# Optimization experiments

Hardware: AMD Instinct MI355X
Metric: run time of the kernel (lower is better)

The kernel has to match this reference:

```python
import jax, jax.numpy as jnp
import numpy as np
from jax import lax

N, E, F, H, B = 16384, 262144, 32, 128, 16
DI, DS, DC, DTR = 256, 16, 4, 8   # Mamba: d_inner=expand*H, d_state, d_conv, dt_rank=ceil(H/16)
NS, NC = 512, 8                   # num_stations, num line colors
EPS = 1e-5


def _forward(node_features, edge_index, batch, W_in, b_in, W_g1, b_g1, W_g2, b_g2,
             W_inproj, conv_w, conv_b, W_xproj, W_dt, b_dt, A_log, D_p, W_out,
             gamma, beta, Wc, bc, Wh, bh, Wt, bt, Wp1, bp1, Wp2, bp2, Wd, bd, Ws, bs):
    def gcn(x, W, b):
        # GCNConv with self-loops and symmetric normalization
        loops = jnp.arange(N)
        s = jnp.concatenate([edge_index[0], loops])
        d = jnp.concatenate([edge_index[1], loops])
        deg = jax.ops.segment_sum(jnp.ones(s.shape[0], x.dtype), d, num_segments=N)
        dinv = jnp.where(deg > 0, lax.rsqrt(deg), 0.0)
        xw = x @ W
        msg = xw[s] * (dinv[s] * dinv[d])[:, None]
        return jax.ops.segment_sum(msg, d, num_segments=N) + b

    h = jax.nn.relu(node_features @ W_in + b_in)
    h = jax.nn.relu(gcn(h, W_g1, b_g1))
    h_gnn = jax.nn.relu(gcn(h, W_g2, b_g2))

    # --- Mamba block over the node sequence (batch dim of 1, seq_len = N) ---
    xz = h_gnn @ W_inproj                      # (N, 2*DI)
    x, z = xz[:, :DI], xz[:, DI:]
    xp = jnp.pad(x, ((DC - 1, 0), (0, 0)))     # causal depthwise conv1d
    xc = conv_b + sum(xp[k:k + N] * conv_w[:, k] for k in range(DC))
    x = jax.nn.silu(xc)
    dbl = x @ W_xproj                          # (N, DTR + 2*DS)
    dt = jax.nn.softplus(dbl[:, :DTR] @ W_dt + b_dt)   # (N, DI)
    Bm = dbl[:, DTR:DTR + DS]                  # (N, DS)
    Cm = dbl[:, DTR + DS:]                     # (N, DS)
    A = -jnp.exp(A_log)                        # (DI, DS)
    dA = jnp.exp(dt[:, :, None] * A[None])     # (N, DI, DS)
    dBx = dt[:, :, None] * Bm[:, None, :] * x[:, :, None]

    def step(hst, t):
        dA_t, dBx_t, C_t = t
        hst = dA_t * hst + dBx_t               # (DI, DS)
        return hst, hst @ C_t                  # (DI,)

    _, ys = lax.scan(step, jnp.zeros((DI, DS), x.dtype), (dA, dBx, Cm))
    y = (ys + D_p * x) * jax.nn.silu(z)
    h_mamba = y @ W_out                        # (N, H)

    # residual + LayerNorm
    hh = h_gnn + h_mamba
    mu = hh.mean(-1, keepdims=True)
    var = ((hh - mu) ** 2).mean(-1, keepdims=True)
    h_final = (hh - mu) * lax.rsqrt(var + EPS) * gamma + beta

    # global_mean_pool per graph
    counts = jax.ops.segment_sum(jnp.ones(N, h_final.dtype), batch, num_segments=B)
    ge = jax.ops.segment_sum(h_final, batch, num_segments=B) / jnp.maximum(counts, 1.0)[:, None]

    # critic + all policy heads, concatenated: [1,4,3,NS,NS,NS,NC]
    return jnp.concatenate([ge @ Wc + bc, ge @ Wh + bh, ge @ Wt + bt,
                            ge @ Wp1 + bp1, ge @ Wp2 + bp2, ge @ Wd + bd,
                            ge @ Ws + bs], axis=-1)


def setup_inputs() -> dict:
    key = jax.random.key(0)
    ks = list(jax.random.split(key, 20))
    p = lambda i, shape, s=0.02: jax.random.normal(ks[i], shape, jnp.float32) * s
    return dict(
        node_features=jax.random.normal(ks[0], (N, F), jnp.float32),
        edge_index=jax.random.randint(ks[1], (2, E), 0, N),
        batch=jnp.sort(jax.random.randint(ks[2], (N,), 0, B)),
        W_in=p(3, (F, H)), b_in=jnp.zeros((H,), jnp.float32),
        W_g1=p(4, (H, H)), b_g1=jnp.zeros((H,), jnp.float32),
        W_g2=p(5, (H, H)), b_g2=jnp.zeros((H,), jnp.float32),
        W_inproj=p(6, (H, 2 * DI)),
        conv_w=p(7, (DI, DC)), conv_b=jnp.zeros((DI,), jnp.float32),
        W_xproj=p(8, (DI, DTR + 2 * DS)),
        W_dt=p(9, (DTR, DI)), b_dt=jnp.full((DI,), -4.0, jnp.float32),
        A_log=jnp.log(jnp.broadcast_to(jnp.arange(1.0, DS + 1.0, dtype=jnp.float32), (DI, DS))),
        D_p=jnp.ones((DI,), jnp.float32),
        W_out=p(10, (DI, H)),
        gamma=jnp.ones((H,), jnp.float32), beta=jnp.zeros((H,), jnp.float32),
        Wc=p(11, (H, 1)), bc=jnp.zeros((1,), jnp.float32),
        Wh=p(12, (H, 4)), bh=jnp.zeros((4,), jnp.float32),
        Wt=p(13, (H, 3)), bt=jnp.zeros((3,), jnp.float32),
        Wp1=p(14, (H, NS)), bp1=jnp.zeros((NS,), jnp.float32),
        Wp2=p(15, (H, NS)), bp2=jnp.zeros((NS,), jnp.float32),
        Wd=p(16, (H, NS)), bd=jnp.zeros((NS,), jnp.float32),
        Ws=p(17, (H, NC)), bs=jnp.zeros((NC,), jnp.float32),
    )


def reference(node_features, edge_index, batch, W_in, b_in, W_g1, b_g1, W_g2, b_g2,
              W_inproj, conv_w, conv_b, W_xproj, W_dt, b_dt, A_log, D_p, W_out,
              gamma, beta, Wc, bc, Wh, bh, Wt, bt, Wp1, bp1, Wp2, bp2, Wd, bd, Ws, bs):
    return _forward(node_features, edge_index, batch, W_in, b_in, W_g1, b_g1, W_g2, b_g2,
                    W_inproj, conv_w, conv_b, W_xproj, W_dt, b_dt, A_log, D_p, W_out,
                    gamma, beta, Wc, bc, Wh, bh, Wt, bt, Wp1, bp1, Wp2, bp2, Wd, bd, Ws, bs)
```

## Files before the change

kernel.cpp:

```cpp
#include <hip/hip_runtime.h>
#include <math.h>

#define NN 16384
#define EE 262144
#define FF 32
#define HH 128
#define BB 16
#define DI 256
#define DS 16
#define DC 4
#define DTR 8
#define OUTW 1552
#define NCH 256
#define CHLEN 64

__device__ __forceinline__ float siluf(float v) { return v / (1.f + __expf(-v)); }
__device__ __forceinline__ float softplusf(float v) {
    return fmaxf(v, 0.f) + __logf(1.f + __expf(-fabsf(v)));
}

__global__ void zero_kernel(int* __restrict__ cnt, float* __restrict__ ge,
                            int* __restrict__ counts) {
    int idx = blockIdx.x * blockDim.x + threadIdx.x;
    if (idx < NN) cnt[idx] = 0;
    if (idx < BB * HH) ge[idx] = 0.f;
    if (idx < BB) counts[idx] = 0;
}

__global__ void deg_kernel(const int* __restrict__ dst, int* __restrict__ cnt) {
    int e = blockIdx.x * blockDim.x + threadIdx.x;
    if (e < EE) atomicAdd(&cnt[dst[e]], 1);
}

__global__ __launch_bounds__(1024) void prefix_kernel(const int* __restrict__ cnt,
                                                      int* __restrict__ rowptr,
                                                      int* __restrict__ cursor,
                                                      float* __restrict__ dinv) {
    __shared__ int part[1024];
    int tid = threadIdx.x;
    int4 c4[4];
#pragma unroll
    for (int j = 0; j < 4; j++) c4[j] = ((const int4*)cnt)[tid * 4 + j];
    int v[16] = {c4[0].x, c4[0].y, c4[0].z, c4[0].w, c4[1].x, c4[1].y, c4[1].z, c4[1].w,
                 c4[2].x, c4[2].y, c4[2].z, c4[2].w, c4[3].x, c4[3].y, c4[3].z, c4[3].w};
    int s = 0;
#pragma unroll
    for (int j = 0; j < 16; j++) s += v[j];
    part[tid] = s;
    __syncthreads();
    for (int off = 1; off < 1024; off <<= 1) {
        int t = (tid >= off) ? part[tid - off] : 0;
        __syncthreads();
        part[tid] += t;
        __syncthreads();
    }
    int running = part[tid] - s;
    int rp[16];
    float dv[16];
#pragma unroll
    for (int j = 0; j < 16; j++) {
        rp[j] = running;
        running += v[j];
        dv[j] = rsqrtf((float)(v[j] + 1));
    }
#pragma unroll
    for (int j = 0; j < 4; j++) {
        int4 r4; r4.x = rp[j*4]; r4.y = rp[j*4+1]; r4.z = rp[j*4+2]; r4.w = rp[j*4+3];
        ((int4*)rowptr)[tid * 4 + j] = r4;
        ((int4*)cursor)[tid * 4 + j] = r4;
        float4 d4; d4.x = dv[j*4]; d4.y = dv[j*4+1]; d4.z = dv[j*4+2]; d4.w = dv[j*4+3];
        ((float4*)dinv)[tid * 4 + j] = d4;
    }
    if (tid == 1023) rowptr[NN] = part[1023];
}

__global__ void scatter_kernel(const int* __restrict__ src, const int* __restrict__ dst,
                               int* __restrict__ cursor, int* __restrict__ col) {
    int e = blockIdx.x * blockDim.x + threadIdx.x;
    if (e < EE) {
        int d = dst[e];
        int pos = atomicAdd(&cursor[d], 1);
        col[pos] = src[e];
    }
}

__global__ __launch_bounds__(256) void gemm_k(const float* __restrict__ A,
                                              const float* __restrict__ B,
                                              const float* __restrict__ bias,
                                              float* __restrict__ C,
                                              int M, int Nn, int K, int act) {
    __shared__ float As[16][68];
    __shared__ float Bs[16][68];
    int tid = threadIdx.x;
    int m0 = blockIdx.y * 64;
    int n0 = blockIdx.x * 64;
    int ty = tid >> 4, tx = tid & 15;
    float acc[4][4] = {{0.f}};
    for (int k0 = 0; k0 < K; k0 += 16) {
#pragma unroll
        for (int l = 0; l < 4; l++) {
            int idx = tid + l * 256;
            int i = idx >> 4, j = idx & 15;
            As[j][i] = A[(size_t)(m0 + i) * K + k0 + j];
        }
#pragma unroll
        for (int l = 0; l < 4; l++) {
            int idx = tid + l * 256;
            int i = idx >> 6, j = idx & 63;
            int n = n0 + j;
            Bs[i][j] = (n < Nn) ? B[(size_t)(k0 + i) * Nn + n] : 0.f;
        }
        __syncthreads();
#pragma unroll
        for (int kk = 0; kk < 16; kk++) {
            float4 a4 = *(const float4*)&As[kk][ty * 4];
            float4 b4 = *(const float4*)&Bs[kk][tx * 4];
            float av[4] = {a4.x, a4.y, a4.z, a4.w};
            float bv[4] = {b4.x, b4.y, b4.z, b4.w};
#pragma unroll
            for (int r = 0; r < 4; r++)
#pragma unroll
                for (int c = 0; c < 4; c++) acc[r][c] = fmaf(av[r], bv[c], acc[r][c]);
        }
        __syncthreads();
    }
    int nb = n0 + tx * 4;
    if (nb < Nn) {
        float4 bi4 = {0.f, 0.f, 0.f, 0.f};
        if (bias) bi4 = *(const float4*)&bias[nb];
#pragma unroll
        for (int r = 0; r < 4; r++) {
            int m = m0 + ty * 4 + r;
            float4 v;
            v.x = acc[r][0] + bi4.x; v.y = acc[r][1] + bi4.y;
            v.z = acc[r][2] + bi4.z; v.w = acc[r][3] + bi4.w;
            if (act == 1) {
                v.x = fmaxf(v.x, 0.f); v.y = fmaxf(v.y, 0.f);
                v.z = fmaxf(v.z, 0.f); v.w = fmaxf(v.w, 0.f);
            }
            *(float4*)&C[(size_t)m * Nn + nb] = v;
        }
    }
}

__global__ __launch_bounds__(512, 4) void gemm_big512(const float* __restrict__ A,
                                                      const float* __restrict__ B,
                                                      float* __restrict__ C,
                                                      int M, int Nn, int K) {
    __shared__ float As[16][132];
    __shared__ float Bs[16][132];
    int tid = threadIdx.x;
    int m0 = blockIdx.y * 128;
    int n0 = blockIdx.x * 128;
    int ty = tid >> 4;
    int tx = tid & 15;
    float acc[4][8] = {{0.f}};
    for (int k0 = 0; k0 < K; k0 += 16) {
        {
            int m = tid >> 2;
            int kc = (tid & 3) * 4;
            float4 a = *(const float4*)&A[(size_t)(m0 + m) * K + k0 + kc];
            As[kc + 0][m] = a.x; As[kc + 1][m] = a.y;
            As[kc + 2][m] = a.z; As[kc + 3][m] = a.w;
        }
        {
            int krow = tid >> 5;
            int c4 = (tid & 31) * 4;
            *(float4*)&Bs[krow][c4] = *(const float4*)&B[(size_t)(k0 + krow) * Nn + n0 + c4];
        }
        __syncthreads();
#pragma unroll
        for (int kk = 0; kk < 16; kk++) {
            float4 a4 = *(const float4*)&As[kk][ty * 4];
            float4 b0 = *(const float4*)&Bs[kk][tx * 4];
            float4 b1 = *(const float4*)&Bs[kk][64 + tx * 4];
            float av[4] = {a4.x, a4.y, a4.z, a4.w};
            float bv[8] = {b0.x, b0.y, b0.z, b0.w, b1.x, b1.y, b1.z, b1.w};
#pragma unroll
            for (int r = 0; r < 4; r++)
#pragma unroll
                for (int c = 0; c < 8; c++) acc[r][c] = fmaf(av[r], bv[c], acc[r][c]);
        }
        __syncthreads();
    }
#pragma unroll
    for (int r = 0; r < 4; r++) {
        int m = m0 + ty * 4 + r;
        float4 v0, v1;
        v0.x = acc[r][0]; v0.y = acc[r][1]; v0.z = acc[r][2]; v0.w = acc[r][3];
        v1.x = acc[r][4]; v1.y = acc[r][5]; v1.z = acc[r][6]; v1.w = acc[r][7];
        *(float4*)&C[(size_t)m * Nn + n0 + tx * 4] = v0;
        *(float4*)&C[(size_t)m * Nn + n0 + 64 + tx * 4] = v1;
    }
}

__global__ __launch_bounds__(256) void gemm_at_dblt(const float* __restrict__ AT,
                                                    const float* __restrict__ B,
                                                    float* __restrict__ dblt) {
    __shared__ float As[16][68];
    __shared__ float Bs[16][68];
    __shared__ float Ct[64][41];
    int tid = threadIdx.x;
    int m0 = blockIdx.x * 64;
    int ty = tid >> 4, tx = tid & 15;
    float acc[4][4] = {{0.f}};
    for (int k0 = 0; k0 < DI; k0 += 16) {
#pragma unroll
        for (int l = 0; l < 4; l++) {
            int idx = tid + l * 256;
            int kk = idx >> 6, i = idx & 63;
            As[kk][i] = AT[(size_t)(k0 + kk) * NN + m0 + i];
        }
#pragma unroll
        for (int l = 0; l < 4; l++) {
            int idx = tid + l * 256;
            int i = idx >> 6, j = idx & 63;
            Bs[i][j] = (j < 40) ? B[(size_t)(k0 + i) * 40 + j] : 0.f;
        }
        __syncthreads();
#pragma unroll
        for (int kk = 0; kk < 16; kk++) {
            float4 a4 = *(const float4*)&As[kk][ty * 4];
            float4 b4 = *(const float4*)&Bs[kk][tx * 4];
            float av[4] = {a4.x, a4.y, a4.z, a4.w};
            float bv[4] = {b4.x, b4.y, b4.z, b4.w};
#pragma unroll
            for (int r = 0; r < 4; r++)
#pragma unroll
                for (int c = 0; c < 4; c++) acc[r][c] = fmaf(av[r], bv[c], acc[r][c]);
        }
        __syncthreads();
    }
    if (tx * 4 < 40) {
#pragma unroll
        for (int r = 0; r < 4; r++) {
            int m = ty * 4 + r;
            Ct[m][tx * 4 + 0] = acc[r][0];
            Ct[m][tx * 4 + 1] = acc[r][1];
            Ct[m][tx * 4 + 2] = acc[r][2];
            Ct[m][tx * 4 + 3] = acc[r][3];
        }
    }
    __syncthreads();
#pragma unroll
    for (int l = 0; l < 10; l++) {
        int idx = tid + l * 256;
        int n = idx >> 6, m = idx & 63;
        dblt[(size_t)n * NN + m0 + m] = Ct[m][n];
    }
}

__global__ __launch_bounds__(256) void gemm_at_ln(const float* __restrict__ AT,
                                                  const float* __restrict__ B,
                                                  const float* __restrict__ hg,
                                                  const float* __restrict__ gamma,
                                                  const float* __restrict__ beta,
                                                  float* __restrict__ out) {
    __shared__ float As[16][36];
    __shared__ float Bs[16][132];
    int tid = threadIdx.x;
    int m0 = blockIdx.x * 32;
    int ty = tid >> 4, tx = tid & 15;
    float acc[2][8] = {{0.f}};
    for (int k0 = 0; k0 < 256; k0 += 16) {
        {
            int idx = tid * 2;
            int kk = idx >> 5, i = idx & 31;
            As[kk][i] = AT[(size_t)(k0 + kk) * NN + m0 + i];
            As[kk][i + 1] = AT[(size_t)(k0 + kk) * NN + m0 + i + 1];
        }
        {
            int krow = tid >> 4;
            int c8 = (tid & 15) * 8;
            const float* bp = &B[(size_t)(k0 + krow) * HH + c8];
            *(float4*)&Bs[krow][c8] = *(const float4*)bp;
            *(float4*)&Bs[krow][c8 + 4] = *(const float4*)(bp + 4);
        }
        __syncthreads();
#pragma unroll
        for (int kk = 0; kk < 16; kk++) {
            float a0 = As[kk][ty * 2];
            float a1 = As[kk][ty * 2 + 1];
            float4 b0 = *(const float4*)&Bs[kk][tx * 4];
            float4 b1 = *(const float4*)&Bs[kk][64 + tx * 4];
            float bv[8] = {b0.x, b0.y, b0.z, b0.w, b1.x, b1.y, b1.z, b1.w};
#pragma unroll
            for (int c = 0; c < 8; c++) {
                acc[0][c] = fmaf(a0, bv[c], acc[0][c]);
                acc[1][c] = fmaf(a1, bv[c], acc[1][c]);
            }
        }
        __syncthreads();
    }
    float4 g0 = *(const float4*)&gamma[tx * 4];
    float4 g1 = *(const float4*)&gamma[64 + tx * 4];
    float4 be0 = *(const float4*)&beta[tx * 4];
    float4 be1 = *(const float4*)&beta[64 + tx * 4];
    float gv[8] = {g0.x, g0.y, g0.z, g0.w, g1.x, g1.y, g1.z, g1.w};
    float bv[8] = {be0.x, be0.y, be0.z, be0.w, be1.x, be1.y, be1.z, be1.w};
#pragma unroll
    for (int r = 0; r < 2; r++) {
        int m = m0 + ty * 2 + r;
        float4 h0 = *(const float4*)&hg[(size_t)m * HH + tx * 4];
        float4 h1 = *(const float4*)&hg[(size_t)m * HH + 64 + tx * 4];
        float v[8] = {acc[r][0] + h0.x, acc[r][1] + h0.y, acc[r][2] + h0.z, acc[r][3] + h0.w,
                      acc[r][4] + h1.x, acc[r][5] + h1.y, acc[r][6] + h1.z, acc[r][7] + h1.w};
        float sum = 0.f;
#pragma unroll
        for (int c = 0; c < 8; c++) sum += v[c];
        sum += __shfl_xor(sum, 1); sum += __shfl_xor(sum, 2);
        sum += __shfl_xor(sum, 4); sum += __shfl_xor(sum, 8);
        float mu = sum * (1.f / 128.f);
        float vs = 0.f;
#pragma unroll
        for (int c = 0; c < 8; c++) { float dd = v[c] - mu; vs += dd * dd; }
        vs += __shfl_xor(vs, 1); vs += __shfl_xor(vs, 2);
        vs += __shfl_xor(vs, 4); vs += __shfl_xor(vs, 8);
        float inv = rsqrtf(vs * (1.f / 128.f) + 1e-5f);
        float4 o0, o1;
        o0.x = (v[0] - mu) * inv * gv[0] + bv[0];
        o0.y = (v[1] - mu) * inv * gv[1] + bv[1];
        o0.z = (v[2] - mu) * inv * gv[2] + bv[2];
        o0.w = (v[3] - mu) * inv * gv[3] + bv[3];
        o1.x = (v[4] - mu) * inv * gv[4] + bv[4];
        o1.y = (v[5] - mu) * inv * gv[5] + bv[5];
        o1.z = (v[6] - mu) * inv * gv[6] + bv[6];
        o1.w = (v[7] - mu) * inv * gv[7] + bv[7];
        *(float4*)&out[(size_t)m * HH + tx * 4] = o0;
        *(float4*)&out[(size_t)m * HH + 64 + tx * 4] = o1;
    }
}

__global__ __launch_bounds__(256) void gcn_gather4(const float* __restrict__ xw,
                                                   const int* __restrict__ rowptr,
                                                   const int* __restrict__ col,
                                                   const float* __restrict__ dinv,
                                                   const float* __restrict__ b,
                                                   float* __restrict__ out) {
    int tid = threadIdx.x;
    int sub = tid & 31;
    int n = blockIdx.x * 8 + (tid >> 5);
    float dn = dinv[n];
    const float4* xw4 = (const float4*)xw;
    float4 a = xw4[(size_t)n * 32 + sub];
    float ws = dn * dn;
    float4 acc;
    acc.x = a.x * ws; acc.y = a.y * ws; acc.z = a.z * ws; acc.w = a.w * ws;
    int beg = rowptr[n], end = rowptr[n + 1];
    int e = beg;
    for (; e + 4 <= end; e += 4) {
        int s0 = col[e], s1 = col[e + 1], s2 = col[e + 2], s3 = col[e + 3];
        float w0 = dinv[s0] * dn, w1 = dinv[s1] * dn;
        float w2 = dinv[s2] * dn, w3 = dinv[s3] * dn;
        float4 v0 = xw4[(size_t)s0 * 32 + sub];
        float4 v1 = xw4[(size_t)s1 * 32 + sub];
        float4 v2 = xw4[(size_t)s2 * 32 + sub];
        float4 v3 = xw4[(size_t)s3 * 32 + sub];
        acc.x = fmaf(v0.x, w0, acc.x); acc.y = fmaf(v0.y, w0, acc.y);
        acc.z = fmaf(v0.z, w0, acc.z); acc.w = fmaf(v0.w, w0, acc.w);
        acc.x = fmaf(v1.x, w1, acc.x); acc.y = fmaf(v1.y, w1, acc.y);
        acc.z = fmaf(v1.z, w1, acc.z); acc.w = fmaf(v1.w, w1, acc.w);
        acc.x = fmaf(v2.x, w2, acc.x); acc.y = fmaf(v2.y, w2, acc.y);
        acc.z = fmaf(v2.z, w2, acc.z); acc.w = fmaf(v2.w, w2, acc.w);
        acc.x = fmaf(v3.x, w3, acc.x); acc.y = fmaf(v3.y, w3, acc.y);
        acc.z = fmaf(v3.z, w3, acc.z); acc.w = fmaf(v3.w, w3, acc.w);
    }
    for (; e < end; e++) {
        int s0 = col[e];
        float w0 = dinv[s0] * dn;
        float4 v0 = xw4[(size_t)s0 * 32 + sub];
        acc.x = fmaf(v0.x, w0, acc.x); acc.y = fmaf(v0.y, w0, acc.y);
        acc.z = fmaf(v0.z, w0, acc.z); acc.w = fmaf(v0.w, w0, acc.w);
    }
    float4 b4 = ((const float4*)b)[sub];
    acc.x = fmaxf(acc.x + b4.x, 0.f);
    acc.y = fmaxf(acc.y + b4.y, 0.f);
    acc.z = fmaxf(acc.z + b4.z, 0.f);
    acc.w = fmaxf(acc.w + b4.w, 0.f);
    ((float4*)out)[(size_t)n * 32 + sub] = acc;
}

__global__ __launch_bounds__(256) void conv_silu_t(const float* __restrict__ xz,
                                                   const float* __restrict__ cw,
                                                   const float* __restrict__ cb,
                                                   float* __restrict__ xst,
                                                   float* __restrict__ szt) {
    __shared__ float tile[67][65];
    int tid = threadIdx.x;
    int t0 = blockIdx.x * 64;
    int c0 = blockIdx.y * 64;
#pragma unroll
    for (int l = 0; l < 17; l++) {
        int idx = tid + l * 256;
        if (idx < 67 * 64) {
            int r = idx >> 6, c = idx & 63;
            int gt = t0 - 3 + r;
            tile[r][c] = (gt >= 0) ? xz[(size_t)gt * 512 + c0 + c] : 0.f;
        }
    }
    __syncthreads();
    int tl = tid & 63;
    int d0 = tid >> 6;
    if (c0 < 256) {
#pragma unroll
        for (int l = 0; l < 16; l++) {
            int dl = d0 + l * 4;
            int dg = c0 + dl;
            float acc = cb[dg];
#pragma unroll
            for (int k = 0; k < DC; k++)
                acc = fmaf(tile[tl + k][dl], cw[dg * DC + k], acc);
            xst[dg * NN + t0 + tl] = siluf(acc);
        }
    } else {
#pragma unroll
        for (int l = 0; l < 16; l++) {
            int dl = d0 + l * 4;
            int dg = c0 - 256 + dl;
            szt[dg * NN + t0 + tl] = siluf(tile[tl + 3][dl]);
        }
    }
}

__global__ __launch_bounds__(256, 6) void scan_phase1(const float* __restrict__ xst,
                                                      const float* __restrict__ dblt,
                                                      const float* __restrict__ A_log,
                                                      const float* __restrict__ W_dt,
                                                      const float* __restrict__ b_dt,
                                                      float* __restrict__ chkP,
                                                      float* __restrict__ chkH) {
    __shared__ float Td[32][68];
    __shared__ float Tx[32][68];
    __shared__ float Bs[16][68];
    __shared__ float D8[8][68];
    int tid = threadIdx.x;
    int wave = tid >> 6, lane = tid & 63;
    int sg = lane & 7, dl = lane >> 3;
    int dblk = blockIdx.x, chunk = blockIdx.y;
    int t0 = chunk * CHLEN;
    int dloc = wave * 8 + dl;
    int d = dblk * 32 + dloc;
    int s0 = 2 * sg;
#pragma unroll
    for (int p = 0; p < 2; p++) {
        int linear = tid + p * 256;
        int row = linear >> 4, c4 = (linear & 15) * 4;
        *(float4*)&Tx[row][c4] = *(const float4*)&xst[(size_t)(dblk * 32 + row) * NN + t0 + c4];
    }
    if (tid < 128) {
        int r = tid >> 4, c4 = (tid & 15) * 4;
        *(float4*)&D8[r][c4] = *(const float4*)&dblt[(size_t)r * NN + t0 + c4];
    }
    {
        int s = tid >> 4, c4 = (tid & 15) * 4;
        *(float4*)&Bs[s][c4] = *(const float4*)&dblt[(size_t)(8 + s) * NN + t0 + c4];
    }
    float A0 = -expf(A_log[d * DS + s0]);
    float A1 = -expf(A_log[d * DS + s0 + 1]);
    __syncthreads();
    {
        int row = tid >> 3;
        int tb = (tid & 7) * 8;
        int dd = dblk * 32 + row;
        float bd = b_dt[dd];
        float wv[8];
#pragma unroll
        for (int j = 0; j < 8; j++) wv[j] = W_dt[j * DI + dd];
#pragma unroll
        for (int j = 0; j < 8; j++) {
            int t = tb + j;
            float acc = bd;
#pragma unroll
            for (int k = 0; k < 8; k++) acc = fmaf(D8[k][t], wv[k], acc);
            Td[row][t] = softplusf(acc);
        }
    }
    __syncthreads();
    float h0 = 0.f, h1 = 0.f, P0 = 1.f, P1 = 1.f;
    for (int i = 0; i < CHLEN; i += 4) {
        float4 d4 = *(const float4*)&Td[dloc][i];
        float4 x4 = *(const float4*)&Tx[dloc][i];
        float4 b04 = *(const float4*)&Bs[s0][i];
        float4 b14 = *(const float4*)&Bs[s0 + 1][i];
#define P1S(U) { float dtv = d4.U; float a0 = __expf(dtv * A0); float a1 = __expf(dtv * A1); \
        float dx = dtv * x4.U; h0 = fmaf(a0, h0, dx * b04.U); h1 = fmaf(a1, h1, dx * b14.U); \
        P0 *= a0; P1 *= a1; }
        P1S(x) P1S(y) P1S(z) P1S(w)
#undef P1S
    }
    int idx = chunk * 4096 + d * DS + s0;
    float2 vP; vP.x = P0; vP.y = P1;
    float2 vH; vH.x = h0; vH.y = h1;
    *(float2*)(chkP + idx) = vP;
    *(float2*)(chkH + idx) = vH;
}

__global__ void scan_phase2(const float* __restrict__ chkP, const float* __restrict__ chkH,
                            float* __restrict__ init) {
    int idx = blockIdx.x * blockDim.x + threadIdx.x;
    float h = 0.f;
    for (int c0 = 0; c0 < NCH; c0 += 8) {
        float p[8], q[8];
#pragma unroll
        for (int j = 0; j < 8; j++) {
            p[j] = chkP[(c0 + j) * 4096 + idx];
            q[j] = chkH[(c0 + j) * 4096 + idx];
        }
#pragma unroll
        for (int j = 0; j < 8; j++) {
            init[(c0 + j) * 4096 + idx] = h;
            h = fmaf(p[j], h, q[j]);
        }
    }
}

__global__ __launch_bounds__(256, 6) void scan_phase3(const float* __restrict__ xst,
                                                      const float* __restrict__ dblt,
                                                      const float* __restrict__ A_log,
                                                      const float* __restrict__ W_dt,
                                                      const float* __restrict__ b_dt,
                                                      const float* __restrict__ init,
                                                      const float* __restrict__ D_p,
                                                      const float* __restrict__ szt,
                                                      float* __restrict__ yt) {
    __shared__ float Td[32][68];
    __shared__ float Tx[32][68];
    __shared__ float Bs[16][68];
    __shared__ float CsD8[16][68];
    int tid = threadIdx.x;
    int wave = tid >> 6, lane = tid & 63;
    int sg = lane & 7, dl = lane >> 3;
    int dblk = blockIdx.x, chunk = blockIdx.y;
    int t0 = chunk * CHLEN;
    int dloc = wave * 8 + dl;
    int d = dblk * 32 + dloc;
    int s0 = 2 * sg;
#pragma unroll
    for (int p = 0; p < 2; p++) {
        int linear = tid + p * 256;
        int row = linear >> 4, c4 = (linear & 15) * 4;
        *(float4*)&Tx[row][c4] = *(const float4*)&xst[(size_t)(dblk * 32 + row) * NN + t0 + c4];
    }
    if (tid < 128) {
        int r = tid >> 4, c4 = (tid & 15) * 4;
        *(float4*)&CsD8[r][c4] = *(const float4*)&dblt[(size_t)r * NN + t0 + c4];
    }
    {
        int s = tid >> 4, c4 = (tid & 15) * 4;
        *(float4*)&Bs[s][c4] = *(const float4*)&dblt[(size_t)(8 + s) * NN + t0 + c4];
    }
    float A0 = -expf(A_log[d * DS + s0]);
    float A1 = -expf(A_log[d * DS + s0 + 1]);
    float Dd = D_p[d];
    float2 ini = *(const float2*)(init + chunk * 4096 + d * DS + s0);
    float h0 = ini.x, h1 = ini.y;
    __syncthreads();
    {
        int row = tid >> 3;
        int tb = (tid & 7) * 8;
        int dd = dblk * 32 + row;
        float bd = b_dt[dd];
        float wv[8];
#pragma unroll
        for (int j = 0; j < 8; j++) wv[j] = W_dt[j * DI + dd];
#pragma unroll
        for (int j = 0; j < 8; j++) {
            int t = tb + j;
            float acc = bd;
#pragma unroll
            for (int k = 0; k < 8; k++) acc = fmaf(CsD8[k][t], wv[k], acc);
            Td[row][t] = softplusf(acc);
        }
    }
    __syncthreads();
    {
        int s = tid >> 4, c4 = (tid & 15) * 4;
        *(float4*)&CsD8[s][c4] = *(const float4*)&dblt[(size_t)(24 + s) * NN + t0 + c4];
    }
    float szv[8];
#pragma unroll
    for (int r = 0; r < 8; r++)
        szv[r] = szt[(size_t)(dblk * 32 + wave * 8 + r) * NN + t0 + lane];
    __syncthreads();
    for (int i = 0; i < CHLEN; i += 4) {
        float4 d4 = *(const float4*)&Td[dloc][i];
        float4 x4 = *(const float4*)&Tx[dloc][i];
        float4 b04 = *(const float4*)&Bs[s0][i];
        float4 b14 = *(const float4*)&Bs[s0 + 1][i];
        float4 c04 = *(const float4*)&CsD8[s0][i];
        float4 c14 = *(const float4*)&CsD8[s0 + 1][i];
        float4 yv;
#define P3S(U) { float dtv = d4.U; float a0 = __expf(dtv * A0); float a1 = __expf(dtv * A1); \
        float dx = dtv * x4.U; h0 = fmaf(a0, h0, dx * b04.U); h1 = fmaf(a1, h1, dx * b14.U); \
        float c = fmaf(h1, c14.U, h0 * c04.U); \
        c += __shfl_xor(c, 1); c += __shfl_xor(c, 2); c += __shfl_xor(c, 4); \
        yv.U = c + Dd * x4.U; }
        P3S(x) P3S(y) P3S(z) P3S(w)
#undef P3S
        if (sg == 0) *(float4*)&Td[dloc][i] = yv;
    }
#pragma unroll
    for (int r = 0; r < 8; r++) {
        int row = wave * 8 + r;
        yt[(size_t)(dblk * 32 + row) * NN + t0 + lane] = Td[row][lane] * szv[r];
    }
}

__global__ void pool_kernel(const float* __restrict__ hf, const int* __restrict__ batch,
                            float* __restrict__ ge, int* __restrict__ counts) {
    int f = threadIdx.x;
    int r0 = blockIdx.x * 64;
    int gcur = batch[r0];
    float acc = 0.f;
    int cnt = 0;
    for (int i = 0; i < 64; i += 4) {
        int r = r0 + i;
        int g0 = batch[r], g3 = batch[r + 3];
        float v0 = hf[(size_t)r * HH + f];
        float v1 = hf[(size_t)(r + 1) * HH + f];
        float v2 = hf[(size_t)(r + 2) * HH + f];
        float v3 = hf[(size_t)(r + 3) * HH + f];
        if (g0 == gcur && g3 == gcur) {
            acc += (v0 + v1) + (v2 + v3);
            cnt += 4;
        } else {
            int gs[4] = {g0, batch[r + 1], batch[r + 2], g3};
            float vs[4] = {v0, v1, v2, v3};
#pragma unroll
            for (int k = 0; k < 4; k++) {
                if (gs[k] != gcur) {
                    atomicAdd(&ge[gcur * HH + f], acc);
                    if (f == 0) atomicAdd(&counts[gcur], cnt);
                    acc = 0.f; cnt = 0; gcur = gs[k];
                }
                acc += vs[k];
                cnt++;
            }
        }
    }
    atomicAdd(&ge[gcur * HH + f], acc);
    if (f == 0) atomicAdd(&counts[gcur], cnt);
}

__global__ void heads_kernel(const float* __restrict__ ge, const int* __restrict__ counts,
                             const float* Wc, const float* bc, const float* Wh, const float* bh,
                             const float* Wt, const float* bt, const float* Wp1, const float* bp1,
                             const float* Wp2, const float* bp2, const float* Wd, const float* bd,
                             const float* Ws, const float* bs, float* __restrict__ out) {
    int col = blockIdx.x * blockDim.x + threadIdx.x;
    int b = blockIdx.y;
    if (col >= OUTW) return;
    const float* W; const float* bi; int lc, w;
    if (col < 1)         { W = Wc;  bi = bc;  lc = col;        w = 1; }
    else if (col < 5)    { W = Wh;  bi = bh;  lc = col - 1;    w = 4; }
    else if (col < 8)    { W = Wt;  bi = bt;  lc = col - 5;    w = 3; }
    else if (col < 520)  { W = Wp1; bi = bp1; lc = col - 8;    w = 512; }
    else if (col < 1032) { W = Wp2; bi = bp2; lc = col - 520;  w = 512; }
    else if (col < 1544) { W = Wd;  bi = bd;  lc = col - 1032; w = 512; }
    else                 { W = Ws;  bi = bs;  lc = col - 1544; w = 8; }
    float scale = 1.f / fmaxf((float)counts[b], 1.f);
    float dot = 0.f;
#pragma unroll 8
    for (int f = 0; f < HH; f++) dot = fmaf(ge[b * HH + f], W[f * w + lc], dot);
    out[(size_t)b * OUTW + col] = bi[lc] + scale * dot;
}

extern "C" void kernel_launch(void* const* d_in, const int* in_sizes, int n_in,
                              void* d_out, int out_size, void* d_ws, size_t ws_size,
                              hipStream_t stream) {
    const float* nf      = (const float*)d_in[0];
    const int*   ei      = (const int*)d_in[1];
    const int*   batch   = (const int*)d_in[2];
    const float* W_in    = (const float*)d_in[3];
    const float* b_in    = (const float*)d_in[4];
    const float* W_g1    = (const float*)d_in[5];
    const float* b_g1    = (const float*)d_in[6];
    const float* W_g2    = (const float*)d_in[7];
    const float* b_g2    = (const float*)d_in[8];
    const float* W_inproj= (const float*)d_in[9];
    const float* conv_w  = (const float*)d_in[10];
    const float* conv_b  = (const float*)d_in[11];
    const float* W_xproj = (const float*)d_in[12];
    const float* W_dt    = (const float*)d_in[13];
    const float* b_dt    = (const float*)d_in[14];
    const float* A_log   = (const float*)d_in[15];
    const float* D_p     = (const float*)d_in[16];
    const float* W_out   = (const float*)d_in[17];
    const float* gamma   = (const float*)d_in[18];
    const float* beta    = (const float*)d_in[19];
    const float* Wc = (const float*)d_in[20]; const float* bc = (const float*)d_in[21];
    const float* Wh = (const float*)d_in[22]; const float* bh = (const float*)d_in[23];
    const float* Wt = (const float*)d_in[24]; const float* bt = (const float*)d_in[25];
    const float* Wp1= (const float*)d_in[26]; const float* bp1= (const float*)d_in[27];
    const float* Wp2= (const float*)d_in[28]; const float* bp2= (const float*)d_in[29];
    const float* Wd = (const float*)d_in[30]; const float* bd = (const float*)d_in[31];
    const float* Ws = (const float*)d_in[32]; const float* bs = (const float*)d_in[33];

    const int* e_src = ei;
    const int* e_dst = ei + EE;

    float* w = (float*)d_ws;
    size_t o = 0;
    float* F0   = w + o; o += (size_t)NN * HH;
    float* F1   = w + o; o += (size_t)NN * HH;
    float* F2   = w + o; o += (size_t)NN * HH;
    float* XZ   = w + o; o += (size_t)NN * 512;
    float* YT   = XZ;
    float* XST  = w + o; o += (size_t)NN * DI;
    float* SZT  = w + o; o += (size_t)NN * DI;
    float* DBLT = w + o; o += (size_t)NN * 40;
    float* GE   = w + o; o += BB * HH;
    float* DINV = w + o; o += NN;
    int* ip = (int*)(w + o);
    int* CNT    = ip; ip += NN;
    int* ROWPTR = ip; ip += NN + 1;
    int* CURSOR = ip; ip += NN;
    int* COL    = ip; ip += EE;
    int* COUNTS = ip; ip += BB;

    float* CHP  = F0;
    float* CHH  = F0 + (size_t)NCH * 4096;
    float* INI  = F1;

    zero_kernel<<<(NN + 255) / 256, 256, 0, stream>>>(CNT, GE, COUNTS);

    deg_kernel<<<EE / 256, 256, 0, stream>>>(e_dst, CNT);
    prefix_kernel<<<1, 1024, 0, stream>>>(CNT, ROWPTR, CURSOR, DINV);
    scatter_kernel<<<EE / 256, 256, 0, stream>>>(e_src, e_dst, CURSOR, COL);

    gemm_k<<<dim3(2, NN / 64), 256, 0, stream>>>(nf, W_in, b_in, F0, NN, HH, FF, 1);
    gemm_k<<<dim3(2, NN / 64), 256, 0, stream>>>(F0, W_g1, nullptr, F1, NN, HH, HH, 0);
    gcn_gather4<<<NN / 8, 256, 0, stream>>>(F1, ROWPTR, COL, DINV, b_g1, F0);
    gemm_k<<<dim3(2, NN / 64), 256, 0, stream>>>(F0, W_g2, nullptr, F1, NN, HH, HH, 0);
    gcn_gather4<<<NN / 8, 256, 0, stream>>>(F1, ROWPTR, COL, DINV, b_g2, F2);

    gemm_big512<<<dim3(4, NN / 128), 512, 0, stream>>>(F2, W_inproj, XZ, NN, 512, HH);
    conv_silu_t<<<dim3(NN / 64, 8), 256, 0, stream>>>(XZ, conv_w, conv_b, XST, SZT);
    gemm_at_dblt<<<NN / 64, 256, 0, stream>>>(XST, W_xproj, DBLT);

    scan_phase1<<<dim3(8, NCH), 256, 0, stream>>>(XST, DBLT, A_log, W_dt, b_dt, CHP, CHH);
    scan_phase2<<<16, 256, 0, stream>>>(CHP, CHH, INI);
    scan_phase3<<<dim3(8, NCH), 256, 0, stream>>>(XST, DBLT, A_log, W_dt, b_dt, INI, D_p, SZT, YT);

    gemm_at_ln<<<NN / 32, 256, 0, stream>>>(YT, W_out, F2, gamma, beta, F0);

    pool_kernel<<<NN / 64, HH, 0, stream>>>(F0, batch, GE, COUNTS);

    heads_kernel<<<dim3((OUTW + 127) / 128, BB), 128, 0, stream>>>(
        GE, COUNTS, Wc, bc, Wh, bh, Wt, bt, Wp1, bp1, Wp2, bp2, Wd, bd, Ws, bs, (float*)d_out);
}
```

Before: 403.7 us.

## Write in_proj output transposed, simplify conv, fuse mean-pool into LayerNorm GEMM

The in_proj GEMM now writes its result in channel-major (transposed) layout, so the causal conv+SiLU becomes a simple row-wise vectorized kernel with no shared-memory transpose tile. Separately, the graph mean-pool is fused into the output-projection+LayerNorm kernel: normalized rows are staged in shared memory and reduced per graph with atomics, which removes the F0 write and re-read and one launch. The transposed stores from the GEMM are float4 but strided by NN, which may be less coalesced, and the fused kernel uses more shared memory.

```diff
diff --git a/kernel.cpp b/kernel.cpp
--- a/kernel.cpp
+++ b/kernel.cpp
@@ -143,10 +143,10 @@
     }
 }
 
-__global__ __launch_bounds__(512, 4) void gemm_big512(const float* __restrict__ A,
-                                                      const float* __restrict__ B,
-                                                      float* __restrict__ C,
-                                                      int M, int Nn, int K) {
+__global__ __launch_bounds__(512, 4) void gemm_big512_t(const float* __restrict__ A,
+                                                        const float* __restrict__ B,
+                                                        float* __restrict__ CT,
+                                                        int M, int Nn, int K) {
     __shared__ float As[16][132];
     __shared__ float Bs[16][132];
     int tid = threadIdx.x;
@@ -184,13 +184,42 @@
         __syncthreads();
     }
 #pragma unroll
-    for (int r = 0; r < 4; r++) {
-        int m = m0 + ty * 4 + r;
-        float4 v0, v1;
-        v0.x = acc[r][0]; v0.y = acc[r][1]; v0.z = acc[r][2]; v0.w = acc[r][3];
-        v1.x = acc[r][4]; v1.y = acc[r][5]; v1.z = acc[r][6]; v1.w = acc[r][7];
-        *(float4*)&C[(size_t)m * Nn + n0 + tx * 4] = v0;
-        *(float4*)&C[(size_t)m * Nn + n0 + 64 + tx * 4] = v1;
+    for (int cc = 0; cc < 4; cc++) {
+        float4 v;
+        v.x = acc[0][cc]; v.y = acc[1][cc]; v.z = acc[2][cc]; v.w = acc[3][cc];
+        *(float4*)&CT[(size_t)(n0 + tx * 4 + cc) * NN + m0 + ty * 4] = v;
+        float4 u;
+        u.x = acc[0][cc + 4]; u.y = acc[1][cc + 4]; u.z = acc[2][cc + 4]; u.w = acc[3][cc + 4];
+        *(float4*)&CT[(size_t)(n0 + 64 + tx * 4 + cc) * NN + m0 + ty * 4] = u;
+    }
+}
+
+__global__ __launch_bounds__(256) void conv_silu_rows(const float* __restrict__ xzt,
+                                                      const float* __restrict__ cw,
+                                                      const float* __restrict__ cb,
+                                                      float* __restrict__ xst,
+                                                      float* __restrict__ szt) {
+    int d = blockIdx.y;
+    int tg = blockIdx.x * 1024 + threadIdx.x * 4;
+    const float* row = xzt + (size_t)d * NN;
+    float4 cur = *(const float4*)&row[tg];
+    if (d < DI) {
+        float4 prev;
+        if (tg == 0) { prev.x = 0.f; prev.y = 0.f; prev.z = 0.f; prev.w = 0.f; }
+        else prev = *(const float4*)&row[tg - 4];
+        float w0 = cw[d * DC + 0], w1 = cw[d * DC + 1];
+        float w2 = cw[d * DC + 2], w3 = cw[d * DC + 3];
+        float b = cb[d];
+        float4 o;
+        o.x = siluf(b + w0 * prev.y + w1 * prev.z + w2 * prev.w + w3 * cur.x);
+        o.y = siluf(b + w0 * prev.z + w1 * prev.w + w2 * cur.x + w3 * cur.y);
+        o.z = siluf(b + w0 * prev.w + w1 * cur.x + w2 * cur.y + w3 * cur.z);
+        o.w = siluf(b + w0 * cur.x + w1 * cur.y + w2 * cur.z + w3 * cur.w);
+        *(float4*)&xst[(size_t)d * NN + tg] = o;
+    } else {
+        float4 o;
+        o.x = siluf(cur.x); o.y = siluf(cur.y); o.z = siluf(cur.z); o.w = siluf(cur.w);
+        *(float4*)&szt[(size_t)(d - DI) * NN + tg] = o;
     }
 }
 
@@ -250,14 +279,18 @@
     }
 }
 
-__global__ __launch_bounds__(256) void gemm_at_ln(const float* __restrict__ AT,
-                                                  const float* __restrict__ B,
-                                                  const float* __restrict__ hg,
-                                                  const float* __restrict__ gamma,
-                                                  const float* __restrict__ beta,
-                                                  float* __restrict__ out) {
+__global__ __launch_bounds__(256) void gemm_at_ln_pool(const float* __restrict__ AT,
+                                                       const float* __restrict__ B,
+                                                       const float* __restrict__ hg,
+                                                       const float* __restrict__ gamma,
+                                                       const float* __restrict__ beta,
+                                                       const int* __restrict__ batch,
+                                                       float* __restrict__ ge,
+                                                       int* __restrict__ counts) {
     __shared__ float As[16][36];
     __shared__ float Bs[16][132];
+    __shared__ float lnb[32][132];
+    __shared__ int gb[32];
     int tid = threadIdx.x;
     int m0 = blockIdx.x * 32;
     int ty = tid >> 4, tx = tid & 15;
@@ -292,6 +325,7 @@
         }
         __syncthreads();
     }
+    if (tid < 32) gb[tid] = batch[m0 + tid];
     float4 g0 = *(const float4*)&gamma[tx * 4];
     float4 g1 = *(const float4*)&gamma[64 + tx * 4];
     float4 be0 = *(const float4*)&beta[tx * 4];
@@ -317,6 +351,7 @@
         vs += __shfl_xor(vs, 1); vs += __shfl_xor(vs, 2);
         vs += __shfl_xor(vs, 4); vs += __shfl_xor(vs, 8);
         float inv = rsqrtf(vs * (1.f / 128.f) + 1e-5f);
+        int lr = ty * 2 + r;
         float4 o0, o1;
         o0.x = (v[0] - mu) * inv * gv[0] + bv[0];
         o0.y = (v[1] - mu) * inv * gv[1] + bv[1];
@@ -326,8 +361,28 @@
         o1.y = (v[5] - mu) * inv * gv[5] + bv[5];
         o1.z = (v[6] - mu) * inv * gv[6] + bv[6];
         o1.w = (v[7] - mu) * inv * gv[7] + bv[7];
-        *(float4*)&out[(size_t)m * HH + tx * 4] = o0;
-        *(float4*)&out[(size_t)m * HH + 64 + tx * 4] = o1;
+        *(float4*)&lnb[lr][tx * 4] = o0;
+        *(float4*)&lnb[lr][64 + tx * 4] = o1;
+    }
+    __syncthreads();
+    if (tid < HH) {
+        int f = tid;
+        int gcur = gb[0];
+        float acc2 = 0.f;
+        int cnt = 0;
+#pragma unroll 4
+        for (int i = 0; i < 32; i++) {
+            int g = gb[i];
+            if (g != gcur) {
+                atomicAdd(&ge[gcur * HH + f], acc2);
+                if (f == 0) atomicAdd(&counts[gcur], cnt);
+                acc2 = 0.f; cnt = 0; gcur = g;
+            }
+            acc2 += lnb[i][f];
+            cnt++;
+        }
+        atomicAdd(&ge[gcur * HH + f], acc2);
+        if (f == 0) atomicAdd(&counts[gcur], cnt);
     }
 }
 
@@ -380,48 +435,6 @@
     ((float4*)out)[(size_t)n * 32 + sub] = acc;
 }
 
-__global__ __launch_bounds__(256) void conv_silu_t(const float* __restrict__ xz,
-                                                   const float* __restrict__ cw,
-                                                   const float* __restrict__ cb,
-                                                   float* __restrict__ xst,
-                                                   float* __restrict__ szt) {
-    __shared__ float tile[67][65];
-    int tid = threadIdx.x;
-    int t0 = blockIdx.x * 64;
-    int c0 = blockIdx.y * 64;
-#pragma unroll
-    for (int l = 0; l < 17; l++) {
-        int idx = tid + l * 256;
-        if (idx < 67 * 64) {
-            int r = idx >> 6, c = idx & 63;
-            int gt = t0 - 3 + r;
-            tile[r][c] = (gt >= 0) ? xz[(size_t)gt * 512 + c0 + c] : 0.f;
-        }
-    }
-    __syncthreads();
-    int tl = tid & 63;
-    int d0 = tid >> 6;
-    if (c0 < 256) {
-#pragma unroll
-        for (int l = 0; l < 16; l++) {
-            int dl = d0 + l * 4;
-            int dg = c0 + dl;
-            float acc = cb[dg];
-#pragma unroll
-            for (int k = 0; k < DC; k++)
-                acc = fmaf(tile[tl + k][dl], cw[dg * DC + k], acc);
-            xst[dg * NN + t0 + tl] = siluf(acc);
-        }
-    } else {
-#pragma unroll
-        for (int l = 0; l < 16; l++) {
-            int dl = d0 + l * 4;
-            int dg = c0 - 256 + dl;
-            szt[dg * NN + t0 + tl] = siluf(tile[tl + 3][dl]);
-        }
-    }
-}
-
 __global__ __launch_bounds__(256, 6) void scan_phase1(const float* __restrict__ xst,
                                                       const float* __restrict__ dblt,
                                                       const float* __restrict__ A_log,
@@ -604,42 +617,6 @@
         int row = wave * 8 + r;
         yt[(size_t)(dblk * 32 + row) * NN + t0 + lane] = Td[row][lane] * szv[r];
     }
-}
-
-__global__ void pool_kernel(const float* __restrict__ hf, const int* __restrict__ batch,
-                            float* __restrict__ ge, int* __restrict__ counts) {
-    int f = threadIdx.x;
-    int r0 = blockIdx.x * 64;
-    int gcur = batch[r0];
-    float acc = 0.f;
-    int cnt = 0;
-    for (int i = 0; i < 64; i += 4) {
-        int r = r0 + i;
-        int g0 = batch[r], g3 = batch[r + 3];
-        float v0 = hf[(size_t)r * HH + f];
-        float v1 = hf[(size_t)(r + 1) * HH + f];
-        float v2 = hf[(size_t)(r + 2) * HH + f];
-        float v3 = hf[(size_t)(r + 3) * HH + f];
-        if (g0 == gcur && g3 == gcur) {
-            acc += (v0 + v1) + (v2 + v3);
-            cnt += 4;
-        } else {
-            int gs[4] = {g0, batch[r + 1], batch[r + 2], g3};
-            float vs[4] = {v0, v1, v2, v3};
-#pragma unroll
-            for (int k = 0; k < 4; k++) {
-                if (gs[k] != gcur) {
-                    atomicAdd(&ge[gcur * HH + f], acc);
-                    if (f == 0) atomicAdd(&counts[gcur], cnt);
-                    acc = 0.f; cnt = 0; gcur = gs[k];
-                }
-                acc += vs[k];
-                cnt++;
-            }
-        }
-    }
-    atomicAdd(&ge[gcur * HH + f], acc);
-    if (f == 0) atomicAdd(&counts[gcur], cnt);
 }
 
 __global__ void heads_kernel(const float* __restrict__ ge, const int* __restrict__ counts,
@@ -704,8 +681,8 @@
     float* F0   = w + o; o += (size_t)NN * HH;
     float* F1   = w + o; o += (size_t)NN * HH;
     float* F2   = w + o; o += (size_t)NN * HH;
-    float* XZ   = w + o; o += (size_t)NN * 512;
-    float* YT   = XZ;
+    float* XZT  = w + o; o += (size_t)NN * 512;
+    float* YT   = XZT;
     float* XST  = w + o; o += (size_t)NN * DI;
     float* SZT  = w + o; o += (size_t)NN * DI;
     float* DBLT = w + o; o += (size_t)NN * 40;
@@ -734,17 +711,15 @@
     gemm_k<<<dim3(2, NN / 64), 256, 0, stream>>>(F0, W_g2, nullptr, F1, NN, HH, HH, 0);
     gcn_gather4<<<NN / 8, 256, 0, stream>>>(F1, ROWPTR, COL, DINV, b_g2, F2);
 
-    gemm_big512<<<dim3(4, NN / 128), 512, 0, stream>>>(F2, W_inproj, XZ, NN, 512, HH);
-    conv_silu_t<<<dim3(NN / 64, 8), 256, 0, stream>>>(XZ, conv_w, conv_b, XST, SZT);
+    gemm_big512_t<<<dim3(4, NN / 128), 512, 0, stream>>>(F2, W_inproj, XZT, NN, 512, HH);
+    conv_silu_rows<<<dim3(NN / 1024, 512), 256, 0, stream>>>(XZT, conv_w, conv_b, XST, SZT);
     gemm_at_dblt<<<NN / 64, 256, 0, stream>>>(XST, W_xproj, DBLT);
 
     scan_phase1<<<dim3(8, NCH), 256, 0, stream>>>(XST, DBLT, A_log, W_dt, b_dt, CHP, CHH);
     scan_phase2<<<16, 256, 0, stream>>>(CHP, CHH, INI);
     scan_phase3<<<dim3(8, NCH), 256, 0, stream>>>(XST, DBLT, A_log, W_dt, b_dt, INI, D_p, SZT, YT);
 
-    gemm_at_ln<<<NN / 32, 256, 0, stream>>>(YT, W_out, F2, gamma, beta, F0);
-
-    pool_kernel<<<NN / 64, HH, 0, stream>>>(F0, batch, GE, COUNTS);
+    gemm_at_ln_pool<<<NN / 32, 256, 0, stream>>>(YT, W_out, F2, gamma, beta, batch, GE, COUNTS);
 
     heads_kernel<<<dim3((OUTW + 127) / 128, BB), 128, 0, stream>>>(
         GE, COUNTS, Wc, bc, Wh, bh, Wt, bt, Wp1, bp1, Wp2, bp2, Wd, bd, Ws, bs, (float*)d_out);
```

Measured after the change: 399.2 us. No clear change (-1.1%).
